# Kernel optimization log

Hardware: AMD Instinct MI355X
Metric: run time of the kernel (lower is better)

The kernel has to match this reference:

```python
import jax, jax.numpy as jnp
import numpy as np

B, S, D, H, HD = 8, 1374, 384, 6, 64
NUM_PATCHES = 1369  # (518 // 14) ** 2
NUM_PREFIX = 5      # 1 cls + 4 registers


def setup_inputs() -> dict:
    key = jax.random.key(0)
    ks = jax.random.split(key, 10)
    init = 0.02  # truncated_normal(0.02) approximated by scaled normal
    x = jax.random.normal(ks[0], (B, S, D), jnp.float32)
    wq = jax.random.truncated_normal(ks[1], -2.0, 2.0, (D, H, HD), jnp.float32) * init
    wk = jax.random.truncated_normal(ks[2], -2.0, 2.0, (D, H, HD), jnp.float32) * init
    wv = jax.random.truncated_normal(ks[3], -2.0, 2.0, (D, H, HD), jnp.float32) * init
    wo = jax.random.truncated_normal(ks[4], -2.0, 2.0, (H, HD, D), jnp.float32) * init
    bq = jnp.zeros((H, HD), jnp.float32)
    bk = jnp.zeros((H, HD), jnp.float32)
    bv = jnp.zeros((H, HD), jnp.float32)
    bo = jnp.zeros((D,), jnp.float32)
    keep_patch_indices = jax.random.randint(ks[5], (B, NUM_PATCHES), 0, NUM_PATCHES).astype(jnp.int64)
    return {"x": x, "wq": wq, "bq": bq, "wk": wk, "bk": bk, "wv": wv, "bv": bv,
            "wo": wo, "bo": bo, "keep_patch_indices": keep_patch_indices, "k_patches": 685}


def reference(x, wq, bq, wk, bk, wv, bv, wo, bo, keep_patch_indices, k_patches):
    # q/k/v projections: DenseGeneral to (heads, head_dim)
    q = jnp.einsum('bsd,dhe->bshe', x, wq) + bq
    k = jnp.einsum('bsd,dhe->bshe', x, wk) + bk
    v = jnp.einsum('bsd,dhe->bshe', x, wv) + bv

    z = jnp.einsum('bqhd,bkhd->bhqk', q / (HD ** 0.5), k)  # [B,H,S,S]
    attn_logits = z  # saved BEFORE masking (used by 'mse' criterion)

    # dynamic scatter mask: patch columns >= k_patches get -inf
    num_selected = keep_patch_indices.shape[1]
    patch_idx = jnp.arange(num_selected)
    indices_to_mask = jnp.where(patch_idx >= k_patches, patch_idx, num_selected) + NUM_PREFIX
    # out-of-bounds indices (== num_selected + NUM_PREFIX) are dropped by JAX scatter semantics
    z = z.at[:, :, :, indices_to_mask].set(-jnp.inf)

    attn_map = jax.nn.softmax(z, axis=-1)
    zo = jnp.einsum('bhqk,bkhd->bqhd', attn_map, v)
    output = jnp.einsum('bqhd,hdo->bqo', zo, wo) + bo  # wo contracts (heads, head_dim)

    # attn_aggregate = ['cls_token','reg_token','patch_token'], zoom_map_criterion='mse'
    am = attn_logits.mean(axis=1)  # mean over heads -> [B,S,S]
    aggs = jnp.stack([
        am[:, 0:1, :].mean(axis=1),      # cls token
        am[:, 1:5, :].mean(axis=1),      # register tokens
        am[:, 5:1374, :].mean(axis=1),   # patch tokens
    ], axis=1)                            # [B,3,S]
    attn_agg = aggs.mean(axis=1)          # [B,S]
    return output, attn_agg
```

## Files before the change

kernel.cpp:

```cpp
#include <hip/hip_runtime.h>
#include <stdint.h>

#define BB 8
#define SS 1374
#define DD 384
#define HH 6
#define HDIM 64
#define MROWS (BB*SS)
#define NPFX 5
#define SPAD 1376

typedef __attribute__((ext_vector_type(8))) short bf16x8;
typedef __attribute__((ext_vector_type(4))) float f32x4;
typedef __attribute__((ext_vector_type(4))) unsigned int u32x4;
typedef u32x4 __attribute__((aligned(4))) u32x4_u;

__device__ __forceinline__ unsigned short f2bf(float f){
  union { float f; unsigned int u; } v; v.f = f;
  return (unsigned short)((v.u + 0x7FFFu + ((v.u >> 16) & 1u)) >> 16);
}
__device__ __forceinline__ float bf2f(unsigned short b){
  union { float f; unsigned int u; } v; v.u = ((unsigned int)b) << 16; return v.f;
}
__device__ __forceinline__ unsigned int pk_bf16(float a, float b){
#if __has_builtin(__builtin_amdgcn_cvt_pk_bf16_f32)
  typedef __attribute__((ext_vector_type(2))) __bf16 bfv2;
  bfv2 p = __builtin_amdgcn_cvt_pk_bf16_f32(a, b);
  union { bfv2 v; unsigned int u; } c; c.v = p; return c.u;
#else
  return (unsigned int)f2bf(a) | ((unsigned int)f2bf(b) << 16);
#endif
}

__device__ __forceinline__ int xcd_remap(int i, int n){
  int q = n >> 3, r = n & 7;
  int x = i & 7, j = i >> 3;
  return (x < r ? x*(q+1) : r*(q+1) + (x - r)*q) + j;
}

__global__ void k_prep(const float* __restrict__ x, const float* __restrict__ wq,
                       const float* __restrict__ wk, const float* __restrict__ wv,
                       const float* __restrict__ wo,
                       unsigned short* __restrict__ xb, float* __restrict__ xbar,
                       unsigned short* __restrict__ wbT, unsigned short* __restrict__ woT){
  int bid = blockIdx.x, t = threadIdx.x;
  if (bid < BB*43){
    int b = bid / 43, ch = bid % 43;
    int d = t;
    int s0 = ch*32, s1 = s0 + 32; if (s1 > SS) s1 = SS;
    float acc = 0.f;
    for (int s = s0; s < s1; ++s){
      float v = x[((size_t)b*SS + s)*DD + d];
      float w = (s == 0) ? (1.f/3.f) : (s < 5) ? (1.f/12.f) : (1.f/4107.f);
      acc += w * v;
      xb[((size_t)b*SS + s)*DD + d] = f2bf(v);
    }
    atomicAdd(&xbar[b*DD + d], acc);
  } else {
    int i = (bid - BB*43)*384 + t;
    if (i < 1152*384){
      int n = i / 384, d = i % 384;
      const float* w = (n < 384) ? wq : (n < 768) ? wk : wv;
      wbT[i] = f2bf(w[(size_t)d*384 + (n % 384)]);
    } else {
      int j = i - 1152*384;
      int n = j / 384, k = j % 384;
      woT[j] = f2bf(wo[(size_t)k*384 + n]);
    }
  }
}

__global__ void k_qbar(const float* __restrict__ xbar, const float* __restrict__ wq,
                       const float* __restrict__ bq, float* __restrict__ qbar){
  __shared__ float xs[DD];
  int b = blockIdx.x, t = threadIdx.x;
  xs[t] = xbar[b*DD + t];
  __syncthreads();
  float acc = bq[t];
  for (int d = 0; d < DD; ++d) acc += xs[d]*wq[(size_t)d*384 + t];
  qbar[b*384 + t] = acc;
}

template<int MODE>
__global__ __launch_bounds__(256) void k_gemm(
    const unsigned short* __restrict__ A, const unsigned short* __restrict__ Bt,
    const float* __restrict__ b0, const float* __restrict__ b1, const float* __restrict__ b2,
    unsigned short* __restrict__ qg, unsigned short* __restrict__ kgp,
    unsigned short* __restrict__ vt, float* __restrict__ out,
    const int* __restrict__ kpat, const float* __restrict__ qbar, float* __restrict__ oagg)
{
  const int NT = (MODE==0) ? 18 : 6;
  int wg = xcd_remap(blockIdx.x, 86*NT);
  int mt = wg / NT, nt = wg % NT;
  const int t = threadIdx.x;
  const int w = t >> 6, lane = t & 63, quad = lane >> 4, l16 = lane & 15;
  const int wm = w >> 1, wn = w & 1;
  const int m0 = mt*128, n0 = nt*64;

  if (MODE == 0 && nt >= 12){
    int s0r_ = m0 % SS;
    int SKv = NPFX + kpat[0]; if (SKv > SS) SKv = SS; if (SKv < 1) SKv = 1;
    int lo = (SKv + 63) & ~63;
    if (s0r_ >= lo && s0r_ + 127 < SS) return;
  }

  constexpr int SMEM_SH = (MODE==0) ? 13824 : 17408;
  __shared__ unsigned short smem[SMEM_SH];
  unsigned short* As = smem;
  unsigned short* Bs = smem + 9216;
  f32x4 acc[4][2];
  #pragma unroll
  for (int i=0;i<4;i++){ acc[i][0] = (f32x4){0,0,0,0}; acc[i][1] = (f32x4){0,0,0,0}; }

  const int ar = t >> 1, akb = (t & 1) * 32;
  int ga = m0 + ar; if (ga > MROWS-1) ga = MROWS-1;
  const unsigned short* ap = A + (size_t)ga*384 + akb;
  const int br = t >> 2, bkb = (t & 3) * 16;
  const unsigned short* bp = Bt + (size_t)(n0 + br)*384 + bkb;

  u32x4 ra[4], rb[2];
  #pragma unroll
  for (int i=0;i<4;i++) ra[i] = *(const u32x4*)(ap + i*8);
  rb[0] = *(const u32x4*)(bp); rb[1] = *(const u32x4*)(bp + 8);

  for (int kc = 0; kc < 6; ++kc){
    __syncthreads();
    #pragma unroll
    for (int i=0;i<4;i++) *(u32x4*)(As + ar*72 + akb + i*8) = ra[i];
    *(u32x4*)(Bs + br*72 + bkb)     = rb[0];
    *(u32x4*)(Bs + br*72 + bkb + 8) = rb[1];
    __syncthreads();
    if (kc + 1 < 6){
      int kn = (kc+1)*64;
      #pragma unroll
      for (int i=0;i<4;i++) ra[i] = *(const u32x4*)(ap + kn + i*8);
      rb[0] = *(const u32x4*)(bp + kn); rb[1] = *(const u32x4*)(bp + kn + 8);
    }
    #pragma unroll
    for (int kh = 0; kh < 2; ++kh){
      bf16x8 af[4], bfr[2];
      #pragma unroll
      for (int rf = 0; rf < 4; ++rf)
        af[rf] = *(const bf16x8*)(As + (wm*64 + rf*16 + l16)*72 + kh*32 + quad*8);
      #pragma unroll
      for (int cf = 0; cf < 2; ++cf)
        bfr[cf] = *(const bf16x8*)(Bs + (wn*32 + cf*16 + l16)*72 + kh*32 + quad*8);
      #pragma unroll
      for (int rf = 0; rf < 4; ++rf)
        #pragma unroll
        for (int cf = 0; cf < 2; ++cf)
          acc[rf][cf] = __builtin_amdgcn_mfma_f32_16x16x32_bf16(af[rf], bfr[cf], acc[rf][cf], 0,0,0);
    }
  }

  const int b0r = m0 / SS, s0r = m0 % SS;
  __syncthreads();
  if (MODE == 1){
    float* CsF = (float*)smem;
    #pragma unroll
    for (int cf = 0; cf < 2; ++cf){
      int e = wn*32 + cf*16 + l16;
      float bias = b0[n0 + e];
      #pragma unroll
      for (int rf = 0; rf < 4; ++rf){
        int rr = wm*64 + rf*16 + quad*4;
        #pragma unroll
        for (int r4 = 0; r4 < 4; ++r4)
          CsF[(rr + r4)*68 + e] = acc[rf][cf][r4] + bias;
      }
    }
    __syncthreads();
    #pragma unroll
    for (int p = 0; p < 8; ++p){
      int r = p*16 + (t >> 4), c = t & 15;
      int rr = m0 + r;
      if (rr < MROWS){
        f32x4 v = *(const f32x4*)(CsF + r*68 + c*4);
        *(f32x4*)(out + (size_t)rr*384 + n0 + c*4) = v;
      }
    }
  } else {
    const int mat = nt / 6, h = nt - mat*6;
    const float* bvp = (mat==0) ? b0 : (mat==1) ? b1 : b2;
    const float vsc = (mat==0) ? 0.125f : 1.f;
    if (mat < 2){
      unsigned short* Cs = As;
      unsigned short* dst = (mat==0) ? qg : kgp;
      #pragma unroll
      for (int cf = 0; cf < 2; ++cf){
        int e = wn*32 + cf*16 + l16;
        float bias = bvp[h*64 + e];
        #pragma unroll
        for (int rf = 0; rf < 4; ++rf){
          int rr = wm*64 + rf*16 + quad*4;
          #pragma unroll
          for (int r4 = 0; r4 < 4; ++r4)
            Cs[(rr + r4)*72 + e] = f2bf((acc[rf][cf][r4] + bias)*vsc);
        }
      }
      __syncthreads();
      #pragma unroll
      for (int p = 0; p < 4; ++p){
        int r = p*32 + (t >> 3), c = t & 7;
        int rr = m0 + r;
        if (rr < MROWS){
          int s = s0r + r, bb = b0r;
          if (s >= SS){ s -= SS; ++bb; }
          u32x4 v = *(const u32x4*)(Cs + r*72 + c*8);
          *(u32x4*)(dst + (((size_t)(bb*HH + h))*SS + s)*64 + c*8) = v;
          if (mat == 1){
            const float* qh = qbar + bb*384 + h*64 + c*8;
            float part = 0.f;
            #pragma unroll
            for (int j = 0; j < 4; ++j){
              unsigned int u = v[j];
              part += qh[2*j]     * bf2f((unsigned short)(u & 0xFFFFu));
              part += qh[2*j + 1] * bf2f((unsigned short)(u >> 16));
            }
            part += __shfl_xor(part, 1);
            part += __shfl_xor(part, 2);
            part += __shfl_xor(part, 4);
            if (c == 0) atomicAdd(oagg + bb*SS + s, part * (1.f/48.f));
          }
        }
      }
    } else {
      unsigned short* CsV = As;
      #pragma unroll
      for (int cf = 0; cf < 2; ++cf){
        int e = wn*32 + cf*16 + l16;
        float bias = bvp[h*64 + e];
        #pragma unroll
        for (int rf = 0; rf < 4; ++rf){
          int rr = wm*64 + rf*16 + quad*4;
          #pragma unroll
          for (int p = 0; p < 2; ++p)
            *(unsigned int*)(CsV + e*136 + rr + p*2) =
                pk_bf16(acc[rf][cf][p*2] + bias, acc[rf][cf][p*2+1] + bias);
        }
      }
      __syncthreads();
      const bool nowrap = (s0r + 127 < SS) && (m0 + 127 < MROWS);
      if (nowrap){
        int e = t >> 2;
        unsigned short* vrow = vt + ((size_t)(b0r*HH + h)*64 + e)*SPAD + s0r;
        #pragma unroll
        for (int i = 0; i < 4; ++i){
          int c = (t & 3)*4 + i;
          u32x4 v = *(const u32x4*)(CsV + e*136 + c*8);
          *(u32x4_u*)(vrow + c*8) = v;
        }
      } else {
        for (int idx = t; idx < 64*64; idx += 256){
          int e = idx >> 6, sp = (idx & 63)*2;
          int rr = m0 + sp;
          if (rr < MROWS){
            int s = s0r + sp, bb = b0r;
            if (s >= SS){ s -= SS; ++bb; }
            *(unsigned int*)(vt + ((size_t)(bb*HH + h)*64 + e)*SPAD + s) =
                *(const unsigned int*)(CsV + e*136 + sp);
          }
        }
      }
    }
  }
}

#define KSTR 72
__global__ __launch_bounds__(256) void k_attn(
    const unsigned short* __restrict__ qg, const unsigned short* __restrict__ kg,
    const unsigned short* __restrict__ vt, unsigned short* __restrict__ zo,
    const int* __restrict__ kpat)
{
  const int NQB = 22;
  int wg = xcd_remap(blockIdx.x, 48*NQB);
  int qb = wg % NQB, bh = wg / NQB;
  int t = threadIdx.x, w = t >> 6, lane = t & 63, quad = lane >> 4, l16 = lane & 15;
  int SK = NPFX + kpat[0]; if (SK > SS) SK = SS; if (SK < 1) SK = 1;
  int niter = (SK + 63) >> 6;
  __shared__ unsigned short Ks[2][64*KSTR];
  __shared__ unsigned short Vs[2][64*KSTR];
  __shared__ unsigned short Ps[4][16*KSTR];
  unsigned short* Pw = &Ps[w][0];
  int q0 = qb*64 + w*16;

  bf16x8 aq[2];
  {
    int qrow = q0 + l16; if (qrow > SS-1) qrow = SS-1;
    const unsigned short* p = qg + ((size_t)bh*SS + qrow)*64;
    aq[0] = *(const bf16x8*)(p + quad*8);
    aq[1] = *(const bf16x8*)(p + 32 + quad*8);
  }
  f32x4 o[4];
  float rsum[4] = {0.f,0.f,0.f,0.f};
  #pragma unroll
  for (int i=0;i<4;i++) o[i] = (f32x4){0.f,0.f,0.f,0.f};

  const int srow = t >> 2, sc = (t & 3) * 16;
  const unsigned short* kbase = kg + ((size_t)bh*SS)*64;
  const unsigned short* vbase = vt + ((size_t)bh*64)*SPAD;
  u32x4 rk[2], rv[2];
  {
    rk[0] = *(const u32x4*)(kbase + (size_t)srow*64 + sc);
    rk[1] = *(const u32x4*)(kbase + (size_t)srow*64 + sc + 8);
    rv[0] = *(const u32x4*)(vbase + (size_t)srow*SPAD + sc);
    rv[1] = *(const u32x4*)(vbase + (size_t)srow*SPAD + sc + 8);
  }

  for (int it = 0; it < niter; ++it){
    int k0 = it*64;
    int cur = it & 1;
    unsigned short* Ksc = &Ks[cur][0];
    unsigned short* Vsc = &Vs[cur][0];
    *(u32x4*)(Ksc + srow*KSTR + sc)     = rk[0];
    *(u32x4*)(Ksc + srow*KSTR + sc + 8) = rk[1];
    *(u32x4*)(Vsc + srow*KSTR + sc)     = rv[0];
    *(u32x4*)(Vsc + srow*KSTR + sc + 8) = rv[1];
    if (it + 1 < niter){
      int kn = k0 + 64;
      int krow = kn + srow; if (krow > SS-1) krow = SS-1;
      rk[0] = *(const u32x4*)(kbase + (size_t)krow*64 + sc);
      rk[1] = *(const u32x4*)(kbase + (size_t)krow*64 + sc + 8);
      rv[0] = *(const u32x4*)(vbase + (size_t)srow*SPAD + kn + sc);
      rv[1] = *(const u32x4*)(vbase + (size_t)srow*SPAD + kn + sc + 8);
    }
    asm volatile("s_waitcnt lgkmcnt(0)" ::: "memory");
    __builtin_amdgcn_s_barrier();

    bool tail = (k0 + 64 > SK);
    #pragma unroll
    for (int ks = 0; ks < 2; ++ks){
      float pp[2][4];
      bf16x8 bkf[2][2];
      #pragma unroll
      for (int ns = 0; ns < 2; ++ns)
        #pragma unroll
        for (int ec = 0; ec < 2; ++ec)
          bkf[ns][ec] = *(const bf16x8*)(Ksc + (ks*32 + 2*l16 + ns)*KSTR + ec*32 + quad*8);
      __builtin_amdgcn_s_setprio(1);
      f32x4 z0 = (f32x4){0.f,0.f,0.f,0.f};
      f32x4 z1 = (f32x4){0.f,0.f,0.f,0.f};
      z0 = __builtin_amdgcn_mfma_f32_16x16x32_bf16(aq[0], bkf[0][0], z0, 0,0,0);
      z0 = __builtin_amdgcn_mfma_f32_16x16x32_bf16(aq[1], bkf[0][1], z0, 0,0,0);
      z1 = __builtin_amdgcn_mfma_f32_16x16x32_bf16(aq[0], bkf[1][0], z1, 0,0,0);
      z1 = __builtin_amdgcn_mfma_f32_16x16x32_bf16(aq[1], bkf[1][1], z1, 0,0,0);
      __builtin_amdgcn_s_setprio(0);
      bool v0 = !tail || (k0 + ks*32 + 2*l16)     < SK;
      bool v1 = !tail || (k0 + ks*32 + 2*l16 + 1) < SK;
      #pragma unroll
      for (int rg = 0; rg < 4; ++rg){
        pp[0][rg] = v0 ? __expf(z0[rg]) : 0.f;
        pp[1][rg] = v1 ? __expf(z1[rg]) : 0.f;
      }
      #pragma unroll
      for (int rg = 0; rg < 4; ++rg){
        rsum[rg] += pp[0][rg] + pp[1][rg];
        *(unsigned int*)(Pw + (quad*4 + rg)*KSTR + ks*32 + 2*l16) =
            pk_bf16(pp[0][rg], pp[1][rg]);
      }
    }
    #pragma unroll
    for (int kc = 0; kc < 2; ++kc){
      bf16x8 ap = *(const bf16x8*)(Pw + l16*KSTR + kc*32 + quad*8);
      __builtin_amdgcn_s_setprio(1);
      #pragma unroll
      for (int nc = 0; nc < 4; ++nc){
        bf16x8 vf = *(const bf16x8*)(Vsc + (nc*16 + l16)*KSTR + kc*32 + quad*8);
        o[nc] = __builtin_amdgcn_mfma_f32_16x16x32_bf16(ap, vf, o[nc], 0,0,0);
      }
      __builtin_amdgcn_s_setprio(0);
    }
  }
  int b = bh / HH, h = bh - (bh/HH)*HH;
  #pragma unroll
  for (int rg = 0; rg < 4; ++rg){
    float s = rsum[rg];
    #pragma unroll
    for (int off = 8; off >= 1; off >>= 1) s += __shfl_xor(s, off);
    int q = q0 + quad*4 + rg;
    if (q >= SS) continue;
    float inv = 1.f / s;
    unsigned short* dst = zo + ((size_t)b*SS + q)*384 + h*64;
    #pragma unroll
    for (int nc = 0; nc < 4; ++nc) dst[nc*16 + l16] = f2bf(o[nc][rg]*inv);
  }
}

extern "C" void kernel_launch(void* const* d_in, const int* in_sizes, int n_in,
                              void* d_out, int out_size, void* d_ws, size_t ws_size,
                              hipStream_t stream){
  const float* x  = (const float*)d_in[0];
  const float* wq = (const float*)d_in[1];
  const float* bq = (const float*)d_in[2];
  const float* wk = (const float*)d_in[3];
  const float* bk = (const float*)d_in[4];
  const float* wv = (const float*)d_in[5];
  const float* bv = (const float*)d_in[6];
  const float* wo = (const float*)d_in[7];
  const float* bo = (const float*)d_in[8];
  const int* kpat = (const int*)d_in[10];
  float* out = (float*)d_out;
  float* out_agg = out + (size_t)MROWS*DD;

  char* ws = (char*)d_ws;
  unsigned short* xb  = (unsigned short*)(ws);
  unsigned short* wbT = (unsigned short*)(ws +  8441856);
  unsigned short* woT = (unsigned short*)(ws +  9326592);
  unsigned short* qg  = (unsigned short*)(ws +  9621504);
  unsigned short* kg  = (unsigned short*)(ws + 18063360);
  unsigned short* vt  = (unsigned short*)(ws + 26505216);
  unsigned short* zo  = (unsigned short*)(ws + 34959360);
  float* xbar         = (float*)(ws + 43401216);
  float* qbar         = (float*)(ws + 43413504);
  (void)in_sizes; (void)n_in; (void)out_size; (void)ws_size;

  hipMemsetAsync(xbar, 0, BB*DD*sizeof(float), stream);
  hipMemsetAsync(out_agg, 0, BB*SS*sizeof(float), stream);
  k_prep<<<BB*43 + 1536, 384, 0, stream>>>(x, wq, wk, wv, wo, xb, xbar, wbT, woT);
  k_qbar<<<BB, DD, 0, stream>>>(xbar, wq, bq, qbar);
  k_gemm<0><<<86*18, 256, 0, stream>>>(xb, wbT, bq, bk, bv, qg, kg, vt, nullptr, kpat, qbar, out_agg);
  k_attn<<<48*22, 256, 0, stream>>>(qg, kg, vt, zo, kpat);
  k_gemm<1><<<86*6, 256, 0, stream>>>(zo, woT, bo, nullptr, nullptr, nullptr, nullptr, nullptr, out, nullptr, nullptr, nullptr);
}
```

Measured before the change: 177.5 us.

## Split prep kernel, add tiled weight transpose, widen qbar grid, lighten GEMM barriers

Weight transposition now runs in its own kernel that stages 32x32 tiles through padded shared memory, so both the fp32 reads and the bf16 writes are coalesced. Before, the transposed reads were strided. The x conversion kernel uses smaller row chunks to spread the work over more blocks. The qbar projection moves from 8 blocks to 48 blocks. In the GEMM, __syncthreads is replaced by an LDS-only waitcnt plus s_barrier, so outstanding global prefetch loads are not drained at each barrier. The cost is one extra kernel launch and more atomics on xbar.

```diff
diff --git a/kernel.cpp b/kernel.cpp
--- a/kernel.cpp
+++ b/kernel.cpp
@@ -38,47 +38,55 @@
   return (x < r ? x*(q+1) : r*(q+1) + (x - r)*q) + j;
 }
 
-__global__ void k_prep(const float* __restrict__ x, const float* __restrict__ wq,
-                       const float* __restrict__ wk, const float* __restrict__ wv,
-                       const float* __restrict__ wo,
-                       unsigned short* __restrict__ xb, float* __restrict__ xbar,
-                       unsigned short* __restrict__ wbT, unsigned short* __restrict__ woT){
-  int bid = blockIdx.x, t = threadIdx.x;
-  if (bid < BB*43){
-    int b = bid / 43, ch = bid % 43;
-    int d = t;
-    int s0 = ch*32, s1 = s0 + 32; if (s1 > SS) s1 = SS;
-    float acc = 0.f;
-    for (int s = s0; s < s1; ++s){
-      float v = x[((size_t)b*SS + s)*DD + d];
-      float w = (s == 0) ? (1.f/3.f) : (s < 5) ? (1.f/12.f) : (1.f/4107.f);
-      acc += w * v;
-      xb[((size_t)b*SS + s)*DD + d] = f2bf(v);
-    }
-    atomicAdd(&xbar[b*DD + d], acc);
-  } else {
-    int i = (bid - BB*43)*384 + t;
-    if (i < 1152*384){
-      int n = i / 384, d = i % 384;
-      const float* w = (n < 384) ? wq : (n < 768) ? wk : wv;
-      wbT[i] = f2bf(w[(size_t)d*384 + (n % 384)]);
-    } else {
-      int j = i - 1152*384;
-      int n = j / 384, k = j % 384;
-      woT[j] = f2bf(wo[(size_t)k*384 + n]);
-    }
+__global__ void k_prep(const float* __restrict__ x, unsigned short* __restrict__ xb,
+                       float* __restrict__ xbar){
+  int b = blockIdx.x / 86, ch = blockIdx.x % 86;
+  int d = threadIdx.x;
+  int s0 = ch*16, s1 = s0 + 16; if (s1 > SS) s1 = SS;
+  float acc = 0.f;
+  for (int s = s0; s < s1; ++s){
+    float v = x[((size_t)b*SS + s)*DD + d];
+    float w = (s == 0) ? (1.f/3.f) : (s < 5) ? (1.f/12.f) : (1.f/4107.f);
+    acc += w * v;
+    xb[((size_t)b*SS + s)*DD + d] = f2bf(v);
+  }
+  atomicAdd(&xbar[b*DD + d], acc);
+}
+
+__global__ __launch_bounds__(256) void k_wtrans(const float* __restrict__ wq,
+    const float* __restrict__ wk, const float* __restrict__ wv, const float* __restrict__ wo,
+    unsigned short* __restrict__ wbT, unsigned short* __restrict__ woT){
+  __shared__ float tile[32][33];
+  int bid = blockIdx.x;
+  int m = bid / 144, tl = bid % 144;
+  int tr = tl / 12, tc = tl % 12;
+  const float* src = (m==0) ? wq : (m==1) ? wk : (m==2) ? wv : wo;
+  unsigned short* dst = (m < 3) ? (wbT + (size_t)m*384*384) : woT;
+  int t = threadIdx.x, c = t & 31, r0 = t >> 5;
+  #pragma unroll
+  for (int p = 0; p < 4; ++p){
+    int r = p*8 + r0;
+    tile[r][c] = src[(size_t)(tr*32 + r)*384 + tc*32 + c];
+  }
+  __syncthreads();
+  #pragma unroll
+  for (int p = 0; p < 4; ++p){
+    int r = p*8 + r0;
+    dst[(size_t)(tc*32 + r)*384 + tr*32 + c] = f2bf(tile[c][r]);
   }
 }
 
 __global__ void k_qbar(const float* __restrict__ xbar, const float* __restrict__ wq,
                        const float* __restrict__ bq, float* __restrict__ qbar){
   __shared__ float xs[DD];
-  int b = blockIdx.x, t = threadIdx.x;
-  xs[t] = xbar[b*DD + t];
+  int b = blockIdx.x / 6, nc = blockIdx.x % 6;
+  int t = threadIdx.x;
+  for (int i = t; i < DD; i += 64) xs[i] = xbar[b*DD + i];
   __syncthreads();
-  float acc = bq[t];
-  for (int d = 0; d < DD; ++d) acc += xs[d]*wq[(size_t)d*384 + t];
-  qbar[b*384 + t] = acc;
+  int n = nc*64 + t;
+  float acc = bq[n];
+  for (int d = 0; d < DD; ++d) acc += xs[d]*wq[(size_t)d*384 + n];
+  qbar[b*384 + n] = acc;
 }
 
 template<int MODE>
@@ -124,12 +132,14 @@
   rb[0] = *(const u32x4*)(bp); rb[1] = *(const u32x4*)(bp + 8);
 
   for (int kc = 0; kc < 6; ++kc){
-    __syncthreads();
+    asm volatile("s_waitcnt lgkmcnt(0)" ::: "memory");
+    __builtin_amdgcn_s_barrier();
     #pragma unroll
     for (int i=0;i<4;i++) *(u32x4*)(As + ar*72 + akb + i*8) = ra[i];
     *(u32x4*)(Bs + br*72 + bkb)     = rb[0];
     *(u32x4*)(Bs + br*72 + bkb + 8) = rb[1];
-    __syncthreads();
+    asm volatile("s_waitcnt lgkmcnt(0)" ::: "memory");
+    __builtin_amdgcn_s_barrier();
     if (kc + 1 < 6){
       int kn = (kc+1)*64;
       #pragma unroll
@@ -416,8 +426,9 @@
 
   hipMemsetAsync(xbar, 0, BB*DD*sizeof(float), stream);
   hipMemsetAsync(out_agg, 0, BB*SS*sizeof(float), stream);
-  k_prep<<<BB*43 + 1536, 384, 0, stream>>>(x, wq, wk, wv, wo, xb, xbar, wbT, woT);
-  k_qbar<<<BB, DD, 0, stream>>>(xbar, wq, bq, qbar);
+  k_prep<<<BB*86, 384, 0, stream>>>(x, xb, xbar);
+  k_wtrans<<<576, 256, 0, stream>>>(wq, wk, wv, wo, wbT, woT);
+  k_qbar<<<48, 64, 0, stream>>>(xbar, wq, bq, qbar);
   k_gemm<0><<<86*18, 256, 0, stream>>>(xb, wbT, bq, bk, bv, qg, kg, vt, nullptr, kpat, qbar, out_agg);
   k_attn<<<48*22, 256, 0, stream>>>(qg, kg, vt, zo, kpat);
   k_gemm<1><<<86*6, 256, 0, stream>>>(zo, woT, bo, nullptr, nullptr, nullptr, nullptr, nullptr, out, nullptr, nullptr, nullptr);
```

Measured after the change: 172.6 us. 2.8% less time.
